# Optimization experiments

Measured on AMD Instinct MI355X. Metric: run time of the kernel, lower is better.

## Reference

```python
import jax, jax.numpy as jnp
import numpy as np

# Kinematic tree from joint_chains: joint j creates child body j.
# parent body index per joint (-1 = ground). Order follows joint_chains:
# [ground_pelvis], [hip_r, hip_l, back],
# [patellofemoral_r, walker_knee_r, acromial_r, patellofemoral_l, walker_knee_l, acromial_l],
# [ankle_r, elbow_r, ankle_l, elbow_l], [subtalar_r, radioulnar_r, subtalar_l, radioulnar_l],
# [mtp_r, radius_hand_r, mtp_l, radius_hand_l]
PARENT = [-1, 0, 0, 0, 1, 1, 3, 2, 2, 3, 5, 6, 8, 9, 10, 11, 12, 13, 14, 15, 16, 17]
NJ = 22      # joints / bodies
NC = 33      # generalized coordinates
B = 131072   # batch of poses


def _axis_rot(axis, a):
    c, s = jnp.cos(a), jnp.sin(a)
    o, z = jnp.ones_like(a), jnp.zeros_like(a)
    if axis == 'X':
        flat = (o, z, z, z, c, -s, z, s, c)
    elif axis == 'Y':
        flat = (c, z, s, z, o, z, -s, z, c)
    else:
        flat = (c, -s, z, s, c, z, z, z, o)
    return jnp.stack(flat, -1).reshape(a.shape + (3, 3))


def _euler_xyz(e):
    # e: (..., 3) Euler angles, convention 'XYZ' -> (..., 3, 3)
    return _axis_rot('X', e[..., 0]) @ _axis_rot('Y', e[..., 1]) @ _axis_rot('Z', e[..., 2])


def setup_inputs() -> dict:
    key = jax.random.key(0)
    ks = jax.random.split(key, 16)
    coords_new = jax.random.normal(ks[0], (B, NC), jnp.float32) * 0.5
    scales_new = jax.random.uniform(ks[1], (B, NJ, 3), jnp.float32, 0.8, 1.2)
    # fixed per-joint frame rotations (proper rotation matrices) and offsets
    X_BpJp_r = _euler_xyz(jax.random.uniform(ks[2], (NJ, 3), jnp.float32, -0.3, 0.3))
    X_BpJp_t = jax.random.normal(ks[3], (NJ, 3, 1), jnp.float32) * 0.1
    X_JcBc_r = _euler_xyz(jax.random.uniform(ks[4], (NJ, 3), jnp.float32, -0.3, 0.3))
    X_BcJc_t = jax.random.normal(ks[5], (NJ, 3, 1), jnp.float32) * 0.1
    X_BBcen_t = jax.random.normal(ks[6], (NJ, 3, 1), jnp.float32) * 0.05
    X_G_r = jnp.eye(3, dtype=jnp.float32)
    X_G_t = jnp.zeros((3, 1), jnp.float32)
    # affine 'spline' coefficients: angle/translation = a * coord + b
    rot_a = jax.random.normal(ks[7], (NJ, 3), jnp.float32) * 0.5
    rot_b = jax.random.normal(ks[8], (NJ, 3), jnp.float32) * 0.1
    trans_a = jax.random.normal(ks[9], (NJ, 3), jnp.float32) * 0.05
    trans_b = jax.random.normal(ks[10], (NJ, 3), jnp.float32) * 0.02
    rot_coord_idx = jax.random.randint(ks[11], (NJ, 3), 0, NC)
    trans_coord_idx = jax.random.randint(ks[12], (NJ, 3), 0, NC)
    return {
        'coords_new': coords_new, 'scales_new': scales_new,
        'X_BpJp_r': X_BpJp_r, 'X_BpJp_t': X_BpJp_t,
        'X_JcBc_r': X_JcBc_r, 'X_BcJc_t': X_BcJc_t, 'X_BBcen_t': X_BBcen_t,
        'X_G_r': X_G_r, 'X_G_t': X_G_t,
        'rot_a': rot_a, 'rot_b': rot_b, 'trans_a': trans_a, 'trans_b': trans_b,
        'rot_coord_idx': rot_coord_idx, 'trans_coord_idx': trans_coord_idx,
    }


def _fk(coords, scales, X_BpJp_r, X_BpJp_t, X_JcBc_r, X_BcJc_t, X_BBcen_t,
        X_G_r, X_G_t, rot_a, rot_b, trans_a, trans_b, rot_idx, trans_idx):
    Bn = coords.shape[0]
    scales = jnp.abs(scales)                       # (B, NJ, 3)
    body_R = [None] * NJ
    body_t = [None] * NJ
    body_pos, joint_pos = [], []
    for j in range(NJ):                            # fixed 22-joint chain
        p = PARENT[j]
        if p < 0:
            scale_p = jnp.ones((Bn, 3, 1), coords.dtype)
            Rp = jnp.broadcast_to(X_G_r, (Bn, 3, 3))
            tp = jnp.broadcast_to(X_G_t, (Bn, 3, 1))
        else:
            scale_p = scales[:, p, :, None]
            Rp, tp = body_R[p], body_t[p]
        scale_c = scales[:, j, :, None]
        # parent-body -> parent-joint frame
        R_GJp = Rp @ X_BpJp_r[j]                   # (B,3,3)
        t_GJp = tp + Rp @ (X_BpJp_t[j] * scale_p)  # (B,3,1)
        if p >= 0:
            joint_pos.append(t_GJp)
        # joint spatial transform driven by coordinates (affine 'splines')
        euler = rot_a[j] * coords[:, rot_idx[j]] + rot_b[j]                 # (B,3)
        t_loc = (trans_a[j] * coords[:, trans_idx[j]] + trans_b[j])[..., None]  # (B,3,1)
        R_loc = _euler_xyz(euler)                  # convention 'XYZ'
        R_GJc = R_GJp @ R_loc
        t_GJc = t_GJp + R_GJp @ (t_loc * scale_p)
        joint_pos.append(t_GJc)
        # child-joint -> child-body frame
        R_GBc = R_GJc @ X_JcBc_r[j]
        t_GBc = t_GJc - R_GBc @ (X_BcJc_t[j] * scale_c)
        body_R[j], body_t[j] = R_GBc, t_GBc
        body_pos.append(t_GBc + R_GBc @ (X_BBcen_t[j] * scale_c))
    bp = jnp.stack(body_pos, 1)[..., 0]            # (B, 22, 3)
    jp = jnp.stack(joint_pos, 1)[..., 0]           # (B, 43, 3)
    return jnp.concatenate([bp, jp], axis=1)       # (B, 65, 3)


def reference(coords_new, scales_new, X_BpJp_r, X_BpJp_t, X_JcBc_r, X_BcJc_t,
              X_BBcen_t, X_G_r, X_G_t, rot_a, rot_b, trans_a, trans_b,
              rot_coord_idx, trans_coord_idx):
    return _fk(coords_new, scales_new, X_BpJp_r, X_BpJp_t, X_JcBc_r, X_BcJc_t,
               X_BBcen_t, X_G_r, X_G_t, rot_a, rot_b, trans_a, trans_b,
               rot_coord_idx, trans_coord_idx)
```

## Files before the change

### kernel.cpp

```cpp
#include <hip/hip_runtime.h>
#include <math.h>

#define NJ 22
#define NC 33
#define BLOCK 256
#define OUTW 195

__global__ __launch_bounds__(BLOCK) void fk_kernel(
    const float* __restrict__ coords,
    const float* __restrict__ scales,
    const float* __restrict__ gBpJp_r,
    const float* __restrict__ gBpJp_t,
    const float* __restrict__ gJcBc_r,
    const float* __restrict__ gBcJc_t,
    const float* __restrict__ gBBcen_t,
    const float* __restrict__ gG_r,
    const float* __restrict__ gG_t,
    const float* __restrict__ grot_a,
    const float* __restrict__ grot_b,
    const float* __restrict__ gtrans_a,
    const float* __restrict__ gtrans_b,
    const int* __restrict__ grot_idx,
    const int* __restrict__ gtrans_idx,
    float* __restrict__ out,
    int Btot)
{
  constexpr int PAR[NJ] = {-1,0,0,0,1,1,3,2,2,3,5,6,8,9,10,11,12,13,14,15,16,17};

  __shared__ alignas(16) float s_coords[BLOCK * NC];
  __shared__ alignas(16) float s_matA[NJ][12];
  __shared__ alignas(16) float s_matC[NJ][12];
  __shared__ alignas(16) float s_vBpJp[NJ][4], s_vBcJc[NJ][4], s_vBBc[NJ][4];
  __shared__ alignas(16) float s_ra[NJ][4], s_rb[NJ][4], s_ta[NJ][4], s_tb[NJ][4];
  __shared__ alignas(16) int   s_ri[NJ][4], s_ti[NJ][4];
  __shared__ alignas(16) float s_Gr[12];
  __shared__ alignas(16) float s_Gt[4];

  const int tid = threadIdx.x;

  if (tid < NJ*9) {
    int j = tid / 9, k = tid - j*9;
    s_matA[j][k] = gBpJp_r[tid];
    s_matC[j][k] = gJcBc_r[tid];
  }
  if (tid < NJ*3) {
    int j = tid / 3, k = tid - j*3;
    s_vBpJp[j][k] = gBpJp_t[tid];
    s_vBcJc[j][k] = gBcJc_t[tid];
    s_vBBc[j][k]  = gBBcen_t[tid];
    s_ra[j][k] = grot_a[tid];
    s_rb[j][k] = grot_b[tid];
    s_ta[j][k] = gtrans_a[tid];
    s_tb[j][k] = gtrans_b[tid];
    s_ri[j][k] = grot_idx[tid];
    s_ti[j][k] = gtrans_idx[tid];
  }
  if (tid < 9) s_Gr[tid] = gG_r[tid];
  if (tid < 3) s_Gt[tid] = gG_t[tid];

  {
    const long long base = (long long)blockIdx.x * (BLOCK * NC);
    const long long lim  = (long long)Btot * NC;
    if (base + BLOCK*NC <= lim) {
      const float4* s4 = reinterpret_cast<const float4*>(coords + base);
      float4* d4 = reinterpret_cast<float4*>(s_coords);
      constexpr int NV4  = (BLOCK*NC)/4;
      constexpr int FULL = NV4 / BLOCK;
      constexpr int REM  = NV4 - FULL*BLOCK;
#pragma unroll
      for (int i = 0; i < FULL; ++i) d4[i*BLOCK + tid] = s4[i*BLOCK + tid];
      if (tid < REM) d4[FULL*BLOCK + tid] = s4[FULL*BLOCK + tid];
    } else {
      for (int k = tid; k < BLOCK*NC; k += BLOCK)
        if (base + k < lim) s_coords[k] = coords[base + k];
    }
  }
  __syncthreads();

  const int b = blockIdx.x * BLOCK + tid;
  if (b >= Btot) return;

  const float* cr = &s_coords[tid * NC];
  float* o = out + (long long)b * OUTW;

  float sv[NJ * 3];
  {
    const float2* s2 = reinterpret_cast<const float2*>(scales + (long long)b * (NJ*3));
#pragma unroll
    for (int i = 0; i < (NJ*3)/2; ++i) {
      const float2 v = s2[i];
      sv[2*i]   = fabsf(v.x);
      sv[2*i+1] = fabsf(v.y);
    }
  }

  float R[NJ][9], T[NJ][3];

#pragma unroll
  for (int j = 0; j < NJ; ++j) {
    const int p = PAR[j];

    const float sc0 = sv[j*3+0];
    const float sc1 = sv[j*3+1];
    const float sc2 = sv[j*3+2];

    float Rp[9], tp0, tp1, tp2, sp0, sp1, sp2;
    if (p < 0) {
#pragma unroll
      for (int i = 0; i < 9; ++i) Rp[i] = s_Gr[i];
      tp0 = s_Gt[0]; tp1 = s_Gt[1]; tp2 = s_Gt[2];
      sp0 = sp1 = sp2 = 1.0f;
    } else {
#pragma unroll
      for (int i = 0; i < 9; ++i) Rp[i] = R[p][i];
      tp0 = T[p][0]; tp1 = T[p][1]; tp2 = T[p][2];
      sp0 = sv[p*3+0]; sp1 = sv[p*3+1]; sp2 = sv[p*3+2];
    }

    float A[9];
#pragma unroll
    for (int i = 0; i < 9; ++i) A[i] = s_matA[j][i];

    float RJp[9];
#pragma unroll
    for (int r = 0; r < 3; ++r) {
#pragma unroll
      for (int c = 0; c < 3; ++c) {
        RJp[r*3+c] = fmaf(Rp[r*3+0], A[c],
                     fmaf(Rp[r*3+1], A[3+c], Rp[r*3+2]*A[6+c]));
      }
    }

    const float v0 = s_vBpJp[j][0]*sp0, v1 = s_vBpJp[j][1]*sp1, v2 = s_vBpJp[j][2]*sp2;
    const float tJp0 = tp0 + fmaf(Rp[0], v0, fmaf(Rp[1], v1, Rp[2]*v2));
    const float tJp1 = tp1 + fmaf(Rp[3], v0, fmaf(Rp[4], v1, Rp[5]*v2));
    const float tJp2 = tp2 + fmaf(Rp[6], v0, fmaf(Rp[7], v1, Rp[8]*v2));
    if (p >= 0) {
      float* jo = o + 66 + 3*(2*j - 1);
      jo[0] = tJp0; jo[1] = tJp1; jo[2] = tJp2;
    }

    const float e0 = fmaf(s_ra[j][0], cr[s_ri[j][0]], s_rb[j][0]);
    const float e1 = fmaf(s_ra[j][1], cr[s_ri[j][1]], s_rb[j][1]);
    const float e2 = fmaf(s_ra[j][2], cr[s_ri[j][2]], s_rb[j][2]);
    const float tl0 = fmaf(s_ta[j][0], cr[s_ti[j][0]], s_tb[j][0]) * sp0;
    const float tl1 = fmaf(s_ta[j][1], cr[s_ti[j][1]], s_tb[j][1]) * sp1;
    const float tl2 = fmaf(s_ta[j][2], cr[s_ti[j][2]], s_tb[j][2]) * sp2;

    float sx, cx, sy, cy, sz, cz;
    __sincosf(e0, &sx, &cx);
    __sincosf(e1, &sy, &cy);
    __sincosf(e2, &sz, &cz);

    float Rl[9];
    Rl[0] = cy*cz;  Rl[1] = -cy*sz;  Rl[2] = sy;
    Rl[3] = fmaf(sx*sy, cz,  cx*sz);
    Rl[4] = fmaf(-sx*sy, sz, cx*cz);
    Rl[5] = -sx*cy;
    Rl[6] = fmaf(-cx*sy, cz, sx*sz);
    Rl[7] = fmaf(cx*sy, sz,  sx*cz);
    Rl[8] = cx*cy;

    float RJc[9];
#pragma unroll
    for (int r = 0; r < 3; ++r) {
#pragma unroll
      for (int c = 0; c < 3; ++c) {
        RJc[r*3+c] = fmaf(RJp[r*3+0], Rl[c],
                     fmaf(RJp[r*3+1], Rl[3+c], RJp[r*3+2]*Rl[6+c]));
      }
    }

    const float tJc0 = tJp0 + fmaf(RJp[0], tl0, fmaf(RJp[1], tl1, RJp[2]*tl2));
    const float tJc1 = tJp1 + fmaf(RJp[3], tl0, fmaf(RJp[4], tl1, RJp[5]*tl2));
    const float tJc2 = tJp2 + fmaf(RJp[6], tl0, fmaf(RJp[7], tl1, RJp[8]*tl2));
    {
      const int q = (j == 0) ? 0 : 2*j;
      float* jo = o + 66 + 3*q;
      jo[0] = tJc0; jo[1] = tJc1; jo[2] = tJc2;
    }

    float C[9];
#pragma unroll
    for (int i = 0; i < 9; ++i) C[i] = s_matC[j][i];
    float* Rj = R[j];
#pragma unroll
    for (int r = 0; r < 3; ++r) {
#pragma unroll
      for (int c = 0; c < 3; ++c) {
        Rj[r*3+c] = fmaf(RJc[r*3+0], C[c],
                    fmaf(RJc[r*3+1], C[3+c], RJc[r*3+2]*C[6+c]));
      }
    }

    const float w0 = s_vBcJc[j][0]*sc0, w1 = s_vBcJc[j][1]*sc1, w2 = s_vBcJc[j][2]*sc2;
    T[j][0] = tJc0 - fmaf(Rj[0], w0, fmaf(Rj[1], w1, Rj[2]*w2));
    T[j][1] = tJc1 - fmaf(Rj[3], w0, fmaf(Rj[4], w1, Rj[5]*w2));
    T[j][2] = tJc2 - fmaf(Rj[6], w0, fmaf(Rj[7], w1, Rj[8]*w2));

    const float u0 = s_vBBc[j][0]*sc0, u1 = s_vBBc[j][1]*sc1, u2 = s_vBBc[j][2]*sc2;
    o[j*3+0] = T[j][0] + fmaf(Rj[0], u0, fmaf(Rj[1], u1, Rj[2]*u2));
    o[j*3+1] = T[j][1] + fmaf(Rj[3], u0, fmaf(Rj[4], u1, Rj[5]*u2));
    o[j*3+2] = T[j][2] + fmaf(Rj[6], u0, fmaf(Rj[7], u1, Rj[8]*u2));
  }
}

extern "C" void kernel_launch(void* const* d_in, const int* in_sizes, int n_in,
                              void* d_out, int out_size, void* d_ws, size_t ws_size,
                              hipStream_t stream) {
  const float* coords   = (const float*)d_in[0];
  const float* scales   = (const float*)d_in[1];
  const float* BpJp_r   = (const float*)d_in[2];
  const float* BpJp_t   = (const float*)d_in[3];
  const float* JcBc_r   = (const float*)d_in[4];
  const float* BcJc_t   = (const float*)d_in[5];
  const float* BBcen_t  = (const float*)d_in[6];
  const float* G_r      = (const float*)d_in[7];
  const float* G_t      = (const float*)d_in[8];
  const float* rot_a    = (const float*)d_in[9];
  const float* rot_b    = (const float*)d_in[10];
  const float* trans_a  = (const float*)d_in[11];
  const float* trans_b  = (const float*)d_in[12];
  const int*   rot_idx  = (const int*)d_in[13];
  const int*   trans_idx= (const int*)d_in[14];
  float* out = (float*)d_out;

  const int Btot = in_sizes[0] / NC;
  const int grid = (Btot + BLOCK - 1) / BLOCK;

  fk_kernel<<<grid, BLOCK, 0, stream>>>(
      coords, scales, BpJp_r, BpJp_t, JcBc_r, BcJc_t, BBcen_t, G_r, G_t,
      rot_a, rot_b, trans_a, trans_b, rot_idx, trans_idx, out, Btot);
}
```

Baseline: 239.1 us.

## Stage outputs in shared memory and flush coalesced per joint group

Each thread now writes its body and joint positions into a shared-memory staging buffer, in four groups of joints. After each group a block barrier runs, and threads copy the buffer out column-wise so that adjacent lanes write adjacent output addresses. This replaces the old per-thread stride-195 scattered stores. The block shrinks to 64 to keep the staging buffer small, and coords are read straight from global memory instead of being staged in shared memory. The cost is extra barriers, a serial 64-row flush loop in which some lanes sit idle, and unstaged coordinate gathers.

```diff
diff --git a/kernel.cpp b/kernel.cpp
--- a/kernel.cpp
+++ b/kernel.cpp
@@ -3,87 +3,173 @@
 
 #define NJ 22
 #define NC 33
-#define BLOCK 256
+#define BLOCK 64
 #define OUTW 195
+#define SBW 55
+
+__device__ __forceinline__ void fk_joint(
+    int j, int BODY0, int JNT0, int NB,
+    const float* __restrict__ crow, const float* sv,
+    float (&R)[NJ][9], float (&T)[NJ][3],
+    float (*SB)[SBW], int tid,
+    const float* s_matA, const float* s_matC,
+    const float* s_vBpJp, const float* s_vBcJc, const float* s_vBBc,
+    const float* s_ra, const float* s_rb, const float* s_ta, const float* s_tb,
+    const int* s_ri, const int* s_ti,
+    const float* s_Gr, const float* s_Gt)
+{
+  constexpr int PAR[NJ] = {-1,0,0,0,1,1,3,2,2,3,5,6,8,9,10,11,12,13,14,15,16,17};
+  const int p = PAR[j];
+
+  const float sc0 = sv[j*3+0], sc1 = sv[j*3+1], sc2 = sv[j*3+2];
+
+  float Rp[9], tp0, tp1, tp2, sp0, sp1, sp2;
+  if (p < 0) {
+#pragma unroll
+    for (int i = 0; i < 9; ++i) Rp[i] = s_Gr[i];
+    tp0 = s_Gt[0]; tp1 = s_Gt[1]; tp2 = s_Gt[2];
+    sp0 = sp1 = sp2 = 1.0f;
+  } else {
+#pragma unroll
+    for (int i = 0; i < 9; ++i) Rp[i] = R[p][i];
+    tp0 = T[p][0]; tp1 = T[p][1]; tp2 = T[p][2];
+    sp0 = sv[p*3+0]; sp1 = sv[p*3+1]; sp2 = sv[p*3+2];
+  }
+
+  float A[9];
+#pragma unroll
+  for (int i = 0; i < 9; ++i) A[i] = s_matA[j*9+i];
+  float RJp[9];
+#pragma unroll
+  for (int r = 0; r < 3; ++r)
+#pragma unroll
+    for (int c = 0; c < 3; ++c)
+      RJp[r*3+c] = fmaf(Rp[r*3+0], A[c],
+                   fmaf(Rp[r*3+1], A[3+c], Rp[r*3+2]*A[6+c]));
+
+  const float v0 = s_vBpJp[j*3+0]*sp0, v1 = s_vBpJp[j*3+1]*sp1, v2 = s_vBpJp[j*3+2]*sp2;
+  const float tJp0 = tp0 + fmaf(Rp[0], v0, fmaf(Rp[1], v1, Rp[2]*v2));
+  const float tJp1 = tp1 + fmaf(Rp[3], v0, fmaf(Rp[4], v1, Rp[5]*v2));
+  const float tJp2 = tp2 + fmaf(Rp[6], v0, fmaf(Rp[7], v1, Rp[8]*v2));
+  if (p >= 0) {
+    const int s = (63 + 6*j) - JNT0 + NB;
+    SB[tid][s+0] = tJp0; SB[tid][s+1] = tJp1; SB[tid][s+2] = tJp2;
+  }
+
+  const float e0 = fmaf(s_ra[j*3+0], crow[s_ri[j*3+0]], s_rb[j*3+0]);
+  const float e1 = fmaf(s_ra[j*3+1], crow[s_ri[j*3+1]], s_rb[j*3+1]);
+  const float e2 = fmaf(s_ra[j*3+2], crow[s_ri[j*3+2]], s_rb[j*3+2]);
+  const float tl0 = fmaf(s_ta[j*3+0], crow[s_ti[j*3+0]], s_tb[j*3+0]) * sp0;
+  const float tl1 = fmaf(s_ta[j*3+1], crow[s_ti[j*3+1]], s_tb[j*3+1]) * sp1;
+  const float tl2 = fmaf(s_ta[j*3+2], crow[s_ti[j*3+2]], s_tb[j*3+2]) * sp2;
+
+  float sx, cx, sy, cy, sz, cz;
+  __sincosf(e0, &sx, &cx);
+  __sincosf(e1, &sy, &cy);
+  __sincosf(e2, &sz, &cz);
+
+  float Rl[9];
+  Rl[0] = cy*cz;  Rl[1] = -cy*sz;  Rl[2] = sy;
+  Rl[3] = fmaf(sx*sy, cz,  cx*sz);
+  Rl[4] = fmaf(-sx*sy, sz, cx*cz);
+  Rl[5] = -sx*cy;
+  Rl[6] = fmaf(-cx*sy, cz, sx*sz);
+  Rl[7] = fmaf(cx*sy, sz,  sx*cz);
+  Rl[8] = cx*cy;
+
+  float RJc[9];
+#pragma unroll
+  for (int r = 0; r < 3; ++r)
+#pragma unroll
+    for (int c = 0; c < 3; ++c)
+      RJc[r*3+c] = fmaf(RJp[r*3+0], Rl[c],
+                   fmaf(RJp[r*3+1], Rl[3+c], RJp[r*3+2]*Rl[6+c]));
+
+  const float tJc0 = tJp0 + fmaf(RJp[0], tl0, fmaf(RJp[1], tl1, RJp[2]*tl2));
+  const float tJc1 = tJp1 + fmaf(RJp[3], tl0, fmaf(RJp[4], tl1, RJp[5]*tl2));
+  const float tJc2 = tJp2 + fmaf(RJp[6], tl0, fmaf(RJp[7], tl1, RJp[8]*tl2));
+  {
+    const int s = (66 + 6*j) - JNT0 + NB;
+    SB[tid][s+0] = tJc0; SB[tid][s+1] = tJc1; SB[tid][s+2] = tJc2;
+  }
+
+  float C[9];
+#pragma unroll
+  for (int i = 0; i < 9; ++i) C[i] = s_matC[j*9+i];
+  float* Rj = R[j];
+#pragma unroll
+  for (int r = 0; r < 3; ++r)
+#pragma unroll
+    for (int c = 0; c < 3; ++c)
+      Rj[r*3+c] = fmaf(RJc[r*3+0], C[c],
+                  fmaf(RJc[r*3+1], C[3+c], RJc[r*3+2]*C[6+c]));
+
+  const float w0 = s_vBcJc[j*3+0]*sc0, w1 = s_vBcJc[j*3+1]*sc1, w2 = s_vBcJc[j*3+2]*sc2;
+  T[j][0] = tJc0 - fmaf(Rj[0], w0, fmaf(Rj[1], w1, Rj[2]*w2));
+  T[j][1] = tJc1 - fmaf(Rj[3], w0, fmaf(Rj[4], w1, Rj[5]*w2));
+  T[j][2] = tJc2 - fmaf(Rj[6], w0, fmaf(Rj[7], w1, Rj[8]*w2));
+
+  const float u0 = s_vBBc[j*3+0]*sc0, u1 = s_vBBc[j*3+1]*sc1, u2 = s_vBBc[j*3+2]*sc2;
+  {
+    const int s = 3*j - BODY0;
+    SB[tid][s+0] = T[j][0] + fmaf(Rj[0], u0, fmaf(Rj[1], u1, Rj[2]*u2));
+    SB[tid][s+1] = T[j][1] + fmaf(Rj[3], u0, fmaf(Rj[4], u1, Rj[5]*u2));
+    SB[tid][s+2] = T[j][2] + fmaf(Rj[6], u0, fmaf(Rj[7], u1, Rj[8]*u2));
+  }
+}
+
+__device__ __forceinline__ void fk_flush(
+    int BODY0, int JNT0, int NB, int S,
+    const float (*SB)[SBW], float* __restrict__ out,
+    long long base_b, int Btot, int tid)
+{
+  if (tid < S) {
+    const int col = (tid < NB) ? (BODY0 + tid) : (JNT0 + tid - NB);
+    for (int r = 0; r < BLOCK; ++r) {
+      const long long row = base_b + r;
+      if (row < Btot) out[row * OUTW + col] = SB[r][tid];
+    }
+  }
+}
 
 __global__ __launch_bounds__(BLOCK) void fk_kernel(
     const float* __restrict__ coords,
     const float* __restrict__ scales,
-    const float* __restrict__ gBpJp_r,
-    const float* __restrict__ gBpJp_t,
-    const float* __restrict__ gJcBc_r,
-    const float* __restrict__ gBcJc_t,
+    const float* __restrict__ gBpJp_r, const float* __restrict__ gBpJp_t,
+    const float* __restrict__ gJcBc_r, const float* __restrict__ gBcJc_t,
     const float* __restrict__ gBBcen_t,
-    const float* __restrict__ gG_r,
-    const float* __restrict__ gG_t,
-    const float* __restrict__ grot_a,
-    const float* __restrict__ grot_b,
-    const float* __restrict__ gtrans_a,
-    const float* __restrict__ gtrans_b,
-    const int* __restrict__ grot_idx,
-    const int* __restrict__ gtrans_idx,
-    float* __restrict__ out,
-    int Btot)
+    const float* __restrict__ gG_r, const float* __restrict__ gG_t,
+    const float* __restrict__ grot_a, const float* __restrict__ grot_b,
+    const float* __restrict__ gtrans_a, const float* __restrict__ gtrans_b,
+    const int* __restrict__ grot_idx, const int* __restrict__ gtrans_idx,
+    float* __restrict__ out, int Btot)
 {
-  constexpr int PAR[NJ] = {-1,0,0,0,1,1,3,2,2,3,5,6,8,9,10,11,12,13,14,15,16,17};
-
-  __shared__ alignas(16) float s_coords[BLOCK * NC];
-  __shared__ alignas(16) float s_matA[NJ][12];
-  __shared__ alignas(16) float s_matC[NJ][12];
-  __shared__ alignas(16) float s_vBpJp[NJ][4], s_vBcJc[NJ][4], s_vBBc[NJ][4];
-  __shared__ alignas(16) float s_ra[NJ][4], s_rb[NJ][4], s_ta[NJ][4], s_tb[NJ][4];
-  __shared__ alignas(16) int   s_ri[NJ][4], s_ti[NJ][4];
-  __shared__ alignas(16) float s_Gr[12];
-  __shared__ alignas(16) float s_Gt[4];
+  __shared__ float SB[BLOCK][SBW];
+  __shared__ float s_matA[NJ*9], s_matC[NJ*9];
+  __shared__ float s_vBpJp[NJ*3], s_vBcJc[NJ*3], s_vBBc[NJ*3];
+  __shared__ float s_ra[NJ*3], s_rb[NJ*3], s_ta[NJ*3], s_tb[NJ*3];
+  __shared__ int   s_ri[NJ*3], s_ti[NJ*3];
+  __shared__ float s_Gr[9], s_Gt[3];
 
   const int tid = threadIdx.x;
 
-  if (tid < NJ*9) {
-    int j = tid / 9, k = tid - j*9;
-    s_matA[j][k] = gBpJp_r[tid];
-    s_matC[j][k] = gJcBc_r[tid];
-  }
-  if (tid < NJ*3) {
-    int j = tid / 3, k = tid - j*3;
-    s_vBpJp[j][k] = gBpJp_t[tid];
-    s_vBcJc[j][k] = gBcJc_t[tid];
-    s_vBBc[j][k]  = gBBcen_t[tid];
-    s_ra[j][k] = grot_a[tid];
-    s_rb[j][k] = grot_b[tid];
-    s_ta[j][k] = gtrans_a[tid];
-    s_tb[j][k] = gtrans_b[tid];
-    s_ri[j][k] = grot_idx[tid];
-    s_ti[j][k] = gtrans_idx[tid];
+  for (int k = tid; k < NJ*9; k += BLOCK) { s_matA[k] = gBpJp_r[k]; s_matC[k] = gJcBc_r[k]; }
+  for (int k = tid; k < NJ*3; k += BLOCK) {
+    s_vBpJp[k] = gBpJp_t[k];  s_vBcJc[k] = gBcJc_t[k];  s_vBBc[k] = gBBcen_t[k];
+    s_ra[k] = grot_a[k];  s_rb[k] = grot_b[k];
+    s_ta[k] = gtrans_a[k]; s_tb[k] = gtrans_b[k];
+    s_ri[k] = grot_idx[k]; s_ti[k] = gtrans_idx[k];
   }
   if (tid < 9) s_Gr[tid] = gG_r[tid];
   if (tid < 3) s_Gt[tid] = gG_t[tid];
-
-  {
-    const long long base = (long long)blockIdx.x * (BLOCK * NC);
-    const long long lim  = (long long)Btot * NC;
-    if (base + BLOCK*NC <= lim) {
-      const float4* s4 = reinterpret_cast<const float4*>(coords + base);
-      float4* d4 = reinterpret_cast<float4*>(s_coords);
-      constexpr int NV4  = (BLOCK*NC)/4;
-      constexpr int FULL = NV4 / BLOCK;
-      constexpr int REM  = NV4 - FULL*BLOCK;
-#pragma unroll
-      for (int i = 0; i < FULL; ++i) d4[i*BLOCK + tid] = s4[i*BLOCK + tid];
-      if (tid < REM) d4[FULL*BLOCK + tid] = s4[FULL*BLOCK + tid];
-    } else {
-      for (int k = tid; k < BLOCK*NC; k += BLOCK)
-        if (base + k < lim) s_coords[k] = coords[base + k];
-    }
-  }
-  __syncthreads();
-
-  const int b = blockIdx.x * BLOCK + tid;
-  if (b >= Btot) return;
-
-  const float* cr = &s_coords[tid * NC];
-  float* o = out + (long long)b * OUTW;
-
-  float sv[NJ * 3];
+  __syncthreads();
+
+  const long long base_b = (long long)blockIdx.x * BLOCK;
+  const long long bb = base_b + tid;
+  const int b = (int)(bb < Btot ? bb : (long long)(Btot - 1));
+  const float* crow = coords + (long long)b * NC;
+
+  float sv[NJ*3];
   {
     const float2* s2 = reinterpret_cast<const float2*>(scales + (long long)b * (NJ*3));
 #pragma unroll
@@ -97,112 +183,35 @@
   float R[NJ][9], T[NJ][3];
 
 #pragma unroll
-  for (int j = 0; j < NJ; ++j) {
-    const int p = PAR[j];
-
-    const float sc0 = sv[j*3+0];
-    const float sc1 = sv[j*3+1];
-    const float sc2 = sv[j*3+2];
-
-    float Rp[9], tp0, tp1, tp2, sp0, sp1, sp2;
-    if (p < 0) {
-#pragma unroll
-      for (int i = 0; i < 9; ++i) Rp[i] = s_Gr[i];
-      tp0 = s_Gt[0]; tp1 = s_Gt[1]; tp2 = s_Gt[2];
-      sp0 = sp1 = sp2 = 1.0f;
-    } else {
-#pragma unroll
-      for (int i = 0; i < 9; ++i) Rp[i] = R[p][i];
-      tp0 = T[p][0]; tp1 = T[p][1]; tp2 = T[p][2];
-      sp0 = sv[p*3+0]; sp1 = sv[p*3+1]; sp2 = sv[p*3+2];
-    }
-
-    float A[9];
-#pragma unroll
-    for (int i = 0; i < 9; ++i) A[i] = s_matA[j][i];
-
-    float RJp[9];
-#pragma unroll
-    for (int r = 0; r < 3; ++r) {
-#pragma unroll
-      for (int c = 0; c < 3; ++c) {
-        RJp[r*3+c] = fmaf(Rp[r*3+0], A[c],
-                     fmaf(Rp[r*3+1], A[3+c], Rp[r*3+2]*A[6+c]));
-      }
-    }
-
-    const float v0 = s_vBpJp[j][0]*sp0, v1 = s_vBpJp[j][1]*sp1, v2 = s_vBpJp[j][2]*sp2;
-    const float tJp0 = tp0 + fmaf(Rp[0], v0, fmaf(Rp[1], v1, Rp[2]*v2));
-    const float tJp1 = tp1 + fmaf(Rp[3], v0, fmaf(Rp[4], v1, Rp[5]*v2));
-    const float tJp2 = tp2 + fmaf(Rp[6], v0, fmaf(Rp[7], v1, Rp[8]*v2));
-    if (p >= 0) {
-      float* jo = o + 66 + 3*(2*j - 1);
-      jo[0] = tJp0; jo[1] = tJp1; jo[2] = tJp2;
-    }
-
-    const float e0 = fmaf(s_ra[j][0], cr[s_ri[j][0]], s_rb[j][0]);
-    const float e1 = fmaf(s_ra[j][1], cr[s_ri[j][1]], s_rb[j][1]);
-    const float e2 = fmaf(s_ra[j][2], cr[s_ri[j][2]], s_rb[j][2]);
-    const float tl0 = fmaf(s_ta[j][0], cr[s_ti[j][0]], s_tb[j][0]) * sp0;
-    const float tl1 = fmaf(s_ta[j][1], cr[s_ti[j][1]], s_tb[j][1]) * sp1;
-    const float tl2 = fmaf(s_ta[j][2], cr[s_ti[j][2]], s_tb[j][2]) * sp2;
-
-    float sx, cx, sy, cy, sz, cz;
-    __sincosf(e0, &sx, &cx);
-    __sincosf(e1, &sy, &cy);
-    __sincosf(e2, &sz, &cz);
-
-    float Rl[9];
-    Rl[0] = cy*cz;  Rl[1] = -cy*sz;  Rl[2] = sy;
-    Rl[3] = fmaf(sx*sy, cz,  cx*sz);
-    Rl[4] = fmaf(-sx*sy, sz, cx*cz);
-    Rl[5] = -sx*cy;
-    Rl[6] = fmaf(-cx*sy, cz, sx*sz);
-    Rl[7] = fmaf(cx*sy, sz,  sx*cz);
-    Rl[8] = cx*cy;
-
-    float RJc[9];
-#pragma unroll
-    for (int r = 0; r < 3; ++r) {
-#pragma unroll
-      for (int c = 0; c < 3; ++c) {
-        RJc[r*3+c] = fmaf(RJp[r*3+0], Rl[c],
-                     fmaf(RJp[r*3+1], Rl[3+c], RJp[r*3+2]*Rl[6+c]));
-      }
-    }
-
-    const float tJc0 = tJp0 + fmaf(RJp[0], tl0, fmaf(RJp[1], tl1, RJp[2]*tl2));
-    const float tJc1 = tJp1 + fmaf(RJp[3], tl0, fmaf(RJp[4], tl1, RJp[5]*tl2));
-    const float tJc2 = tJp2 + fmaf(RJp[6], tl0, fmaf(RJp[7], tl1, RJp[8]*tl2));
-    {
-      const int q = (j == 0) ? 0 : 2*j;
-      float* jo = o + 66 + 3*q;
-      jo[0] = tJc0; jo[1] = tJc1; jo[2] = tJc2;
-    }
-
-    float C[9];
-#pragma unroll
-    for (int i = 0; i < 9; ++i) C[i] = s_matC[j][i];
-    float* Rj = R[j];
-#pragma unroll
-    for (int r = 0; r < 3; ++r) {
-#pragma unroll
-      for (int c = 0; c < 3; ++c) {
-        Rj[r*3+c] = fmaf(RJc[r*3+0], C[c],
-                    fmaf(RJc[r*3+1], C[3+c], RJc[r*3+2]*C[6+c]));
-      }
-    }
-
-    const float w0 = s_vBcJc[j][0]*sc0, w1 = s_vBcJc[j][1]*sc1, w2 = s_vBcJc[j][2]*sc2;
-    T[j][0] = tJc0 - fmaf(Rj[0], w0, fmaf(Rj[1], w1, Rj[2]*w2));
-    T[j][1] = tJc1 - fmaf(Rj[3], w0, fmaf(Rj[4], w1, Rj[5]*w2));
-    T[j][2] = tJc2 - fmaf(Rj[6], w0, fmaf(Rj[7], w1, Rj[8]*w2));
-
-    const float u0 = s_vBBc[j][0]*sc0, u1 = s_vBBc[j][1]*sc1, u2 = s_vBBc[j][2]*sc2;
-    o[j*3+0] = T[j][0] + fmaf(Rj[0], u0, fmaf(Rj[1], u1, Rj[2]*u2));
-    o[j*3+1] = T[j][1] + fmaf(Rj[3], u0, fmaf(Rj[4], u1, Rj[5]*u2));
-    o[j*3+2] = T[j][2] + fmaf(Rj[6], u0, fmaf(Rj[7], u1, Rj[8]*u2));
-  }
+  for (int j = 0; j <= 4; ++j)
+    fk_joint(j, 0, 66, 15, crow, sv, R, T, SB, tid, s_matA, s_matC,
+             s_vBpJp, s_vBcJc, s_vBBc, s_ra, s_rb, s_ta, s_tb, s_ri, s_ti, s_Gr, s_Gt);
+  __syncthreads();
+  fk_flush(0, 66, 15, 42, SB, out, base_b, Btot, tid);
+  __syncthreads();
+
+#pragma unroll
+  for (int j = 5; j <= 10; ++j)
+    fk_joint(j, 15, 93, 18, crow, sv, R, T, SB, tid, s_matA, s_matC,
+             s_vBpJp, s_vBcJc, s_vBBc, s_ra, s_rb, s_ta, s_tb, s_ri, s_ti, s_Gr, s_Gt);
+  __syncthreads();
+  fk_flush(15, 93, 18, 54, SB, out, base_b, Btot, tid);
+  __syncthreads();
+
+#pragma unroll
+  for (int j = 11; j <= 16; ++j)
+    fk_joint(j, 33, 129, 18, crow, sv, R, T, SB, tid, s_matA, s_matC,
+             s_vBpJp, s_vBcJc, s_vBBc, s_ra, s_rb, s_ta, s_tb, s_ri, s_ti, s_Gr, s_Gt);
+  __syncthreads();
+  fk_flush(33, 129, 18, 54, SB, out, base_b, Btot, tid);
+  __syncthreads();
+
+#pragma unroll
+  for (int j = 17; j <= 21; ++j)
+    fk_joint(j, 51, 165, 15, crow, sv, R, T, SB, tid, s_matA, s_matC,
+             s_vBpJp, s_vBcJc, s_vBBc, s_ra, s_rb, s_ta, s_tb, s_ri, s_ti, s_Gr, s_Gt);
+  __syncthreads();
+  fk_flush(51, 165, 15, 45, SB, out, base_b, Btot, tid);
 }
 
 extern "C" void kernel_launch(void* const* d_in, const int* in_sizes, int n_in,
```

Result: no change. 234.7 us (-1.9%).
